# Optimization experiments

Measured on AMD Instinct MI355X. Metric: run time of the kernel, lower is better.

Reference implementation:

```python
import jax, jax.numpy as jnp
import numpy as np
from jax import lax

B, T = 32, 20
H, E, A, V = 256, 512, 256, 10000
GH, GW, D = 32, 32, 256          # info spatial grid and channel dim
P = GH * GW                      # num_pixels = 1024
IN_FLAT = P * D                  # 262144
REL = 128 * 128                  # 16384
LSTM_IN = E + D + H              # input to gate linears (x = [word, att_feat], then cat h)


def setup_inputs() -> dict:
    key = jax.random.key(0)
    ks = iter(jax.random.split(key, 40))
    def W(shape, scale=0.05):
        return jax.random.normal(next(ks), shape, jnp.float32) * scale
    inp = {}
    inp["info"] = jax.random.normal(next(ks), (B, GH, GW, D), jnp.float32)
    inp["relation"] = jax.random.normal(next(ks), (B, 128, 128), jnp.float32)
    inp["captions"] = jax.random.randint(next(ks), (B, T), 0, V)
    lens = jax.random.randint(next(ks), (B, 1), 5, T + 1).at[0, 0].set(T)
    inp["captions_lens"] = lens
    # embedding + attention
    inp["emb"] = W((V, E), 0.1)
    inp["W_enc"] = W((D, A)); inp["b_enc"] = jnp.zeros((A,), jnp.float32)
    inp["W_dec"] = W((H, A)); inp["b_dec"] = jnp.zeros((A,), jnp.float32)
    inp["W_full"] = W((A,));  inp["b_full"] = jnp.zeros((), jnp.float32)
    # MSLSTM cell (5 gate linears + mlp)
    for g in ("i", "f", "o", "g1", "g2"):
        inp[f"W_{g}"] = W((LSTM_IN, H)); inp[f"b_{g}"] = jnp.zeros((H,), jnp.float32)
    inp["W_mlp"] = W((2 * H, H)); inp["b_mlp"] = jnp.zeros((H,), jnp.float32)
    # f_beta, fc, init-state linears
    inp["W_beta"] = W((H, D)); inp["b_beta"] = jnp.zeros((D,), jnp.float32)
    inp["W_fc"] = W((H, V), 0.1); inp["b_fc"] = jnp.zeros((V,), jnp.float32)
    inp["W_ih"] = W((IN_FLAT, H), 0.005); inp["b_ih"] = jnp.zeros((H,), jnp.float32)
    inp["W_ic"] = W((IN_FLAT, H), 0.005); inp["b_ic"] = jnp.zeros((H,), jnp.float32)
    inp["W_iC"] = W((REL, H), 0.01);      inp["b_iC"] = jnp.zeros((H,), jnp.float32)
    return inp


def reference(info, relation, captions, captions_lens, emb,
              W_enc, b_enc, W_dec, b_dec, W_full, b_full,
              W_i, b_i, W_f, b_f, W_o, b_o, W_g1, b_g1, W_g2, b_g2,
              W_mlp, b_mlp, W_beta, b_beta, W_fc, b_fc,
              W_ih, b_ih, W_ic, b_ic, W_iC, b_iC):
    Bsz = captions.shape[0]
    info_f = info.reshape(Bsz, P, D)
    rel_f = relation.reshape(Bsz, REL)
    lens = captions_lens[:, 0]
    order = jnp.argsort(-lens)                      # sort descending by length
    lens = lens[order]
    caps = captions[order]
    info_f = info_f[order]
    rel_f = rel_f[order]
    sent_len = lens - 1
    Tm = captions.shape[1] - 1                      # static: max len forced to T in setup

    words = emb[caps]                               # (B, T, E)
    flat = info_f.reshape(Bsz, -1)                  # (B, P*D)
    h = flat @ W_ih + b_ih
    c = flat @ W_ic + b_ic
    C = rel_f @ W_iC + b_iC
    att1 = info_f @ W_enc + b_enc                   # (B, P, A) -- invariant over t

    def step(carry, xs):
        h, c, C = carry
        word, t = xs                                # word: (B, E)
        att2 = h @ W_dec + b_dec                    # (B, A)
        e = jax.nn.relu(att1 + att2[:, None, :]) @ W_full + b_full   # (B, P)
        alpha = jax.nn.softmax(e, axis=1)
        awf = jnp.einsum('bpd,bp->bd', info_f, alpha)                # (B, D)
        # note: gate=sigmoid(f_beta(h)) is computed in torch but its product is unused
        x = jnp.concatenate([word, awf, h], axis=1)  # cat([x, h]) with x=[word, awf]
        i = jax.nn.sigmoid(x @ W_i + b_i)
        f = jax.nn.sigmoid(x @ W_f + b_f)
        o = jax.nn.sigmoid(x @ W_o + b_o)
        g1 = jnp.tanh(x @ W_g1 + b_g1)
        g2 = jnp.tanh(x @ W_g2 + b_g2)
        new_c = f * c + i * g1
        new_C = f * C + i * g2
        new_h = o * jnp.tanh(jnp.concatenate([new_c, new_C], axis=1) @ W_mlp + b_mlp)
        pred = new_h @ W_fc + b_fc                  # dropout in eval mode = identity
        mask = (sent_len > t)[:, None].astype(pred.dtype)
        return (new_h, new_c, new_C), (pred * mask, alpha * mask)

    words_t = jnp.swapaxes(words[:, :Tm], 0, 1)     # (Tm, B, E)
    (_, (preds, alphas)) = lax.scan(step, (h, c, C), (words_t, jnp.arange(Tm)))
    predictions = jnp.swapaxes(preds, 0, 1)         # (B, Tm, V)
    alphas = jnp.swapaxes(alphas, 0, 1)             # (B, Tm, P)
    return predictions, alphas, order
```

## Files before the change

### kernel.cpp

```cpp
#include <hip/hip_runtime.h>
#include <math.h>

#define Bz 32
#define Tz 20
#define TMz 19
#define Vz 10000
#define INFLAT 262144
#define RELSZ 16384
#define NBLK 512

#define WS_PH     0
#define WS_PC     4194304
#define WS_ATT1H  0
#define WS_INFOH  4194304
#define WS_EXPE   8388608
#define WS_ZSUM   8421376
#define WS_AWF    8421888
#define WS_GSP    8430080
#define WS_HST    8593920
#define WS_CST0   8602112
#define WS_CSTB0  8610304
#define WS_CST1   8618496
#define WS_CSTB1  8626688
#define WS_AT2P   8634880
#define WS_INTS   8700416
#define WS_PCHC   8701440
#define WS_WG16   8701440
#define WS_WFC16  9750016
#define WS_END_WFC (9750016 + 1280000)

__device__ __forceinline__ float sigm(float x) { return 1.0f / (1.0f + expf(-x)); }

__device__ __forceinline__ unsigned short f2bf(float f) {
    unsigned int x = __float_as_uint(f);
    unsigned int r = (x + 0x7fffu + ((x >> 16) & 1u)) >> 16;
    return (unsigned short)r;
}
__device__ __forceinline__ float bfl(unsigned int u) { return __uint_as_float(u << 16); }
__device__ __forceinline__ float bfh(unsigned int u) { return __uint_as_float(u & 0xffff0000u); }

__device__ __forceinline__ float agload(const float* p) {
    return __hip_atomic_load(p, __ATOMIC_RELAXED, __HIP_MEMORY_SCOPE_AGENT);
}
__device__ __forceinline__ void agstore(float* p, float v) {
    __hip_atomic_store(p, v, __ATOMIC_RELAXED, __HIP_MEMORY_SCOPE_AGENT);
}
__device__ __forceinline__ int agloadi(const int* p) {
    return __hip_atomic_load(p, __ATOMIC_RELAXED, __HIP_MEMORY_SCOPE_AGENT);
}
__device__ __forceinline__ void agstorei(int* p, int v) {
    __hip_atomic_store(p, v, __ATOMIC_RELAXED, __HIP_MEMORY_SCOPE_AGENT);
}
__device__ __forceinline__ void agadd(float* p, float v) {
    __hip_atomic_fetch_add(p, v, __ATOMIC_RELAXED, __HIP_MEMORY_SCOPE_AGENT);
}

__device__ __forceinline__ void gbar(int* slots, int* root, int gen) {
    asm volatile("s_waitcnt vmcnt(0)" ::: "memory");
    __syncthreads();
    if (blockIdx.x == 0) {
        int i0 = threadIdx.x, i1 = threadIdx.x + 256;
        if (i0 != 0) {
            while (agloadi(&slots[i0]) < gen) __builtin_amdgcn_s_sleep(1);
        }
        while (agloadi(&slots[i1]) < gen) __builtin_amdgcn_s_sleep(1);
        __syncthreads();
        if (threadIdx.x == 0) agstorei(root, gen);
    } else if (threadIdx.x == 0) {
        agstorei(&slots[blockIdx.x], gen);
        while (agloadi(root) < gen) __builtin_amdgcn_s_sleep(2);
    }
    __syncthreads();
    asm volatile("" ::: "memory");
}

__global__ void k_sort(const int* __restrict__ lens, float* __restrict__ out_order,
                       int* __restrict__ ord, int* __restrict__ sentlen, int* __restrict__ barmem) {
    if (threadIdx.x == 0 && blockIdx.x == 0) {
        for (int i = 0; i < 64 + NBLK; ++i) barmem[i] = 0;
        int l[Bz]; bool used[Bz];
        for (int b = 0; b < Bz; ++b) { l[b] = lens[b]; used[b] = false; }
        for (int i = 0; i < Bz; ++i) {
            int best = -1;
            for (int j = 0; j < Bz; ++j)
                if (!used[j] && (best < 0 || l[j] > l[best])) best = j;
            used[best] = true;
            ord[i] = best;
            sentlen[i] = l[best] - 1;
            out_order[i] = (float)best;
        }
    }
}

__global__ __launch_bounds__(256) void k_gemv2(const float* __restrict__ X, const int* __restrict__ ord,
                                               const float* __restrict__ W1, const float* __restrict__ W2,
                                               float* __restrict__ p1, float* __restrict__ p2) {
    __shared__ __align__(16) float xsT[512 * 36];
    __shared__ int ords[32];
    int tid = threadIdx.x;
    size_t k0 = (size_t)blockIdx.x * 512;

    if (tid < 32) ords[tid] = ord[tid];
    __syncthreads();

    for (int idx = tid; idx < 4096; idx += 256) {
        int b = idx >> 7, kq = idx & 127;
        float4 v = *(const float4*)&X[(size_t)ords[b] * INFLAT + k0 + kq * 4];
        xsT[(kq * 4 + 0) * 36 + b] = v.x;
        xsT[(kq * 4 + 1) * 36 + b] = v.y;
        xsT[(kq * 4 + 2) * 36 + b] = v.z;
        xsT[(kq * 4 + 3) * 36 + b] = v.w;
    }
    __syncthreads();

    float ah[32], ac[32];
#pragma unroll
    for (int b = 0; b < 32; ++b) { ah[b] = 0.f; ac[b] = 0.f; }

    const float* w1p = W1 + k0 * 256 + tid;
    const float* w2p = W2 + k0 * 256 + tid;
#pragma unroll 4
    for (int k = 0; k < 512; ++k) {
        float w1 = w1p[(size_t)k * 256];
        float w2 = w2p[(size_t)k * 256];
        const float4* xr = (const float4*)&xsT[k * 36];
#pragma unroll
        for (int bq = 0; bq < 8; ++bq) {
            float4 x4 = xr[bq];
            ah[bq * 4 + 0] += x4.x * w1; ac[bq * 4 + 0] += x4.x * w2;
            ah[bq * 4 + 1] += x4.y * w1; ac[bq * 4 + 1] += x4.y * w2;
            ah[bq * 4 + 2] += x4.z * w1; ac[bq * 4 + 2] += x4.z * w2;
            ah[bq * 4 + 3] += x4.w * w1; ac[bq * 4 + 3] += x4.w * w2;
        }
    }
#pragma unroll
    for (int b = 0; b < 32; ++b) {
        size_t o = ((size_t)blockIdx.x * 32 + b) * 256 + tid;
        p1[o] = ah[b];
        p2[o] = ac[b];
    }
}

__global__ __launch_bounds__(256) void k_gemvC(const float* __restrict__ R, const int* __restrict__ ord,
                                               const float* __restrict__ W, float* __restrict__ p) {
    __shared__ float xs[32 * 128];
    __shared__ int ords[32];
    int tid = threadIdx.x, bx = blockIdx.x;
    if (tid < 32) ords[tid] = ord[tid];
    __syncthreads();
    int k0 = bx * 128;
    for (int idx = tid; idx < 32 * 128; idx += 256) {
        int b = idx >> 7, kk = idx & 127;
        xs[idx] = R[(size_t)ords[b] * RELSZ + k0 + kk];
    }
    __syncthreads();
    float acc[32];
#pragma unroll
    for (int b = 0; b < 32; ++b) acc[b] = 0.f;
    for (int kk = 0; kk < 128; ++kk) {
        float w = W[(size_t)(k0 + kk) * 256 + tid];
#pragma unroll
        for (int b = 0; b < 32; ++b) acc[b] += xs[b * 128 + kk] * w;
    }
#pragma unroll
    for (int b = 0; b < 32; ++b) p[((size_t)bx * 32 + b) * 256 + tid] = acc[b];
}

__global__ __launch_bounds__(256) void k_reduce3(const float* __restrict__ ph, const float* __restrict__ pc,
                                                 const float* __restrict__ pC,
                                                 const float* __restrict__ b_ih, const float* __restrict__ b_ic,
                                                 const float* __restrict__ b_iC,
                                                 float* __restrict__ hst, float* __restrict__ cst,
                                                 float* __restrict__ Cst) {
    int which = blockIdx.x >> 5, b = blockIdx.x & 31, j = threadIdx.x;
    if (which == 0) {
        float s0 = b_ih[j], s1 = 0.f, s2 = 0.f, s3 = 0.f;
        for (int c = 0; c < 512; c += 4) {
            s0 += ph[((size_t)((c + 0) * 32 + b)) * 256 + j];
            s1 += ph[((size_t)((c + 1) * 32 + b)) * 256 + j];
            s2 += ph[((size_t)((c + 2) * 32 + b)) * 256 + j];
            s3 += ph[((size_t)((c + 3) * 32 + b)) * 256 + j];
        }
        hst[b * 256 + j] = s0 + s1 + s2 + s3;
    } else if (which == 1) {
        float s0 = b_ic[j], s1 = 0.f, s2 = 0.f, s3 = 0.f;
        for (int c = 0; c < 512; c += 4) {
            s0 += pc[((size_t)((c + 0) * 32 + b)) * 256 + j];
            s1 += pc[((size_t)((c + 1) * 32 + b)) * 256 + j];
            s2 += pc[((size_t)((c + 2) * 32 + b)) * 256 + j];
            s3 += pc[((size_t)((c + 3) * 32 + b)) * 256 + j];
        }
        cst[b * 256 + j] = s0 + s1 + s2 + s3;
    } else {
        float s0 = b_iC[j], s1 = 0.f, s2 = 0.f, s3 = 0.f;
        for (int c = 0; c < 128; c += 4) {
            s0 += pC[((size_t)((c + 0) * 32 + b)) * 256 + j];
            s1 += pC[((size_t)((c + 1) * 32 + b)) * 256 + j];
            s2 += pC[((size_t)((c + 2) * 32 + b)) * 256 + j];
            s3 += pC[((size_t)((c + 3) * 32 + b)) * 256 + j];
        }
        Cst[b * 256 + j] = s0 + s1 + s2 + s3;
    }
}

__global__ __launch_bounds__(256) void k_init2(const float* __restrict__ hst, const float* __restrict__ W_dec,
                                               float* __restrict__ at2p, float* __restrict__ awf,
                                               float* __restrict__ zsum) {
    __shared__ __align__(16) float hs[8192];
    int tid = threadIdx.x;
    for (int i = blockIdx.x * 256 + tid; i < 8192; i += 1024) awf[i] = 0.f;
    if (blockIdx.x == 0 && tid < 32) zsum[tid] = 0.f;
    for (int i = tid; i < 2048; i += 256) ((float4*)hs)[i] = ((const float4*)hst)[i];
    __syncthreads();
    int col = blockIdx.x * 64 + (tid & 63), bg = tid >> 6;
    float acc[8] = {0.f,0.f,0.f,0.f,0.f,0.f,0.f,0.f};
    for (int k = 0; k < 256; ++k) {
        float w = W_dec[(size_t)k * 256 + col];
#pragma unroll
        for (int bi = 0; bi < 8; ++bi) acc[bi] += hs[(bg * 8 + bi) * 256 + k] * w;
    }
#pragma unroll
    for (int bi = 0; bi < 8; ++bi) {
        int b = bg * 8 + bi;
        at2p[((size_t)(b * 8 + 0)) * 256 + col] = acc[bi];
#pragma unroll
        for (int ct = 1; ct < 8; ++ct) at2p[((size_t)(b * 8 + ct)) * 256 + col] = 0.f;
    }
}

__global__ __launch_bounds__(256) void k_wfc16(const float* __restrict__ W_fc,
                                               unsigned short* __restrict__ wfcT16) {
    __shared__ unsigned short tile[16 * 256];
    int tid = threadIdx.x;
    int c0 = blockIdx.x * 16;
    for (int p = 0; p < 16; ++p) {
        int r = p * 16 + (tid >> 4);
        int c = tid & 15;
        tile[c * 256 + r] = f2bf(W_fc[(size_t)r * Vz + c0 + c]);
    }
    __syncthreads();
    unsigned int* dst = (unsigned int*)wfcT16 + (size_t)c0 * 128;
    const unsigned int* src = (const unsigned int*)tile;
    for (int i = tid; i < 2048; i += 256) dst[i] = src[i];
}

__global__ __launch_bounds__(256) void k_wg16(const float* __restrict__ W_i, const float* __restrict__ W_f,
                                              const float* __restrict__ W_o, const float* __restrict__ W_g1,
                                              const float* __restrict__ W_g2,
                                              unsigned short* __restrict__ wg16) {
    __shared__ unsigned short tile[16 * 1024];
    int tid = threadIdx.x;
    int g = blockIdx.x >> 4;
    int c0 = (blockIdx.x & 15) * 16;
    const float* Wg = (g == 0) ? W_i : (g == 1) ? W_f : (g == 2) ? W_o : (g == 3) ? W_g1 : W_g2;
    for (int p = 0; p < 64; ++p) {
        int r = p * 16 + (tid >> 4);
        int c = tid & 15;
        tile[c * 1024 + r] = f2bf(Wg[(size_t)r * 256 + c0 + c]);
    }
    __syncthreads();
    unsigned int* dst = (unsigned int*)wg16 + ((size_t)(g * 256 + c0)) * 512;
    const unsigned int* src = (const unsigned int*)tile;
    for (int i = tid; i < 8192; i += 256) dst[i] = src[i];
}

__global__ __launch_bounds__(256) void k_att1(const float* __restrict__ info, const int* __restrict__ ord,
                                              const float* __restrict__ W, const float* __restrict__ bias,
                                              unsigned short* __restrict__ att1h,
                                              unsigned short* __restrict__ infoh) {
    __shared__ __align__(16) float xsT[256 * 36];
    int tid = threadIdx.x;
    int r0 = blockIdx.x * 32;
    int b = r0 >> 10, p0 = r0 & 1023;
    const float* src = info + (size_t)ord[b] * INFLAT + (size_t)p0 * 256;
    for (int idx = tid; idx < 2048; idx += 256) {
        int r = idx >> 6, kq = idx & 63;
        float4 v = *(const float4*)&src[r * 256 + kq * 4];
        xsT[(kq * 4 + 0) * 36 + r] = v.x;
        xsT[(kq * 4 + 1) * 36 + r] = v.y;
        xsT[(kq * 4 + 2) * 36 + r] = v.z;
        xsT[(kq * 4 + 3) * 36 + r] = v.w;
    }
    __syncthreads();
#pragma unroll 4
    for (int r = 0; r < 32; ++r)
        infoh[(size_t)(r0 + r) * 256 + tid] = f2bf(xsT[tid * 36 + r]);
    float acc[32];
#pragma unroll
    for (int r = 0; r < 32; ++r) acc[r] = 0.f;
    for (int k = 0; k < 256; ++k) {
        float w = W[k * 256 + tid];
        const float4* xr = (const float4*)&xsT[k * 36];
#pragma unroll
        for (int rq = 0; rq < 8; ++rq) {
            float4 x4 = xr[rq];
            acc[rq * 4 + 0] += x4.x * w;
            acc[rq * 4 + 1] += x4.y * w;
            acc[rq * 4 + 2] += x4.z * w;
            acc[rq * 4 + 3] += x4.w * w;
        }
    }
    float bj = bias[tid];
#pragma unroll
    for (int r = 0; r < 32; ++r)
        att1h[(size_t)(r0 + r) * 256 + tid] = f2bf(acc[r] + bj);
}

struct KArgs {
    const float *info, *emb, *W_dec, *b_dec, *W_full, *b_full;
    const float *b_i, *b_f, *b_o, *b_g1, *b_g2;
    const float *W_mlp, *b_mlp, *W_fc, *b_fc;
    const int *caps;
    const unsigned short *att1h, *infoh, *wfcT16, *wg16;
    float *expe, *zsum, *awf, *gsp, *hst, *cst0, *Cst0, *cst1, *Cst1, *at2p;
    const int *ord, *slp;
    int *root, *slots;
    float *out_pred, *out_alpha;
};

__device__ void pred_task2(const KArgs& a, unsigned short* hb, int tile, int tm1) {
    int tid = threadIdx.x;
    for (int i = tid; i < 8192; i += 256) hb[i] = f2bf(agload(&a.hst[i]));
    __syncthreads();
    int col = tile * 64 + (tid & 63), bg = tid >> 6;
    if (col >= Vz) return;
    float acc[8] = {0.f, 0.f, 0.f, 0.f, 0.f, 0.f, 0.f, 0.f};
    if (a.wfcT16) {
        const uint4* wcol = (const uint4*)(a.wfcT16 + (size_t)col * 256);
#pragma unroll 4
        for (int q = 0; q < 32; ++q) {
            uint4 u = wcol[q];
            float w0 = bfl(u.x), w1 = bfh(u.x), w2 = bfl(u.y), w3 = bfh(u.y);
            float w4 = bfl(u.z), w5 = bfh(u.z), w6 = bfl(u.w), w7 = bfh(u.w);
#pragma unroll
            for (int bi = 0; bi < 8; ++bi) {
                uint4 hv = *(const uint4*)&hb[(bg * 8 + bi) * 256 + q * 8];
                acc[bi] += bfl(hv.x) * w0 + bfh(hv.x) * w1 + bfl(hv.y) * w2 + bfh(hv.y) * w3
                         + bfl(hv.z) * w4 + bfh(hv.z) * w5 + bfl(hv.w) * w6 + bfh(hv.w) * w7;
            }
        }
    } else {
        for (int jq = 0; jq < 64; ++jq) {
            float w0 = a.W_fc[(size_t)(jq * 4 + 0) * Vz + col];
            float w1 = a.W_fc[(size_t)(jq * 4 + 1) * Vz + col];
            float w2 = a.W_fc[(size_t)(jq * 4 + 2) * Vz + col];
            float w3 = a.W_fc[(size_t)(jq * 4 + 3) * Vz + col];
#pragma unroll
            for (int bi = 0; bi < 8; ++bi) {
                uint2 u = *(const uint2*)&hb[(bg * 8 + bi) * 256 + jq * 4];
                acc[bi] += bfl(u.x) * w0 + bfh(u.x) * w1 + bfl(u.y) * w2 + bfh(u.y) * w3;
            }
        }
    }
    float bv = a.b_fc[col];
#pragma unroll
    for (int bi = 0; bi < 8; ++bi) {
        int b = bg * 8 + bi;
        float r = (a.slp[b] > tm1) ? (acc[bi] + bv) : 0.f;
        a.out_pred[((size_t)b * TMz + tm1) * Vz + col] = r;
    }
}

__global__ __launch_bounds__(256, 2) void k_steps(KArgs a) {
    __shared__ __align__(16) unsigned char smem[81920];
    unsigned char* attB = smem;
    unsigned char* infB = smem + 32768;
    float* F = (float*)(smem + 65536);
    unsigned short* S16 = (unsigned short*)(smem + 65536);

    int bid = blockIdx.x, tid = threadIdx.x;
    int b = bid >> 4, sub = bid & 15;
    int gen = 0;

    {
        const unsigned short* ag = a.att1h + (size_t)(b * 1024 + sub * 64) * 256;
        const unsigned short* ig = a.infoh + (size_t)(b * 1024 + sub * 64) * 256;
        for (int idx = tid; idx < 2048; idx += 256) {
            int r = idx >> 5, qc = idx & 31;
            uint4 v = *(const uint4*)(ag + (size_t)r * 256 + qc * 8);
            *(uint4*)(attB + r * 512 + ((qc ^ (r & 7)) << 4)) = v;
            uint4 w2 = *(const uint4*)(ig + (size_t)r * 256 + qc * 8);
            *(uint4*)(infB + idx * 16) = w2;
        }
    }
    __syncthreads();

    for (int t = 0; t < TMz; ++t) {
        {
            float v = a.b_dec[tid];
#pragma unroll
            for (int ct = 0; ct < 8; ++ct) v += agload(&a.at2p[((size_t)(b * 8 + ct)) * 256 + tid]);
            F[tid] = v;
            F[256 + tid] = a.W_full[tid];
            __syncthreads();
            int pl = tid & 63, kq = tid >> 6;
            float part = 0.f;
#pragma unroll
            for (int q = 0; q < 8; ++q) {
                int c = kq * 8 + q;
                uint4 u = *(const uint4*)(attB + pl * 512 + ((c ^ (pl & 7)) << 4));
                const float* A = F + kq * 64 + q * 8;
                const float* W = F + 256 + kq * 64 + q * 8;
                part += fmaxf(bfl(u.x) + A[0], 0.f) * W[0];
                part += fmaxf(bfh(u.x) + A[1], 0.f) * W[1];
                part += fmaxf(bfl(u.y) + A[2], 0.f) * W[2];
                part += fmaxf(bfh(u.y) + A[3], 0.f) * W[3];
                part += fmaxf(bfl(u.z) + A[4], 0.f) * W[4];
                part += fmaxf(bfh(u.z) + A[5], 0.f) * W[5];
                part += fmaxf(bfl(u.w) + A[6], 0.f) * W[6];
                part += fmaxf(bfh(u.w) + A[7], 0.f) * W[7];
            }
            F[512 + kq * 64 + pl] = part;
            __syncthreads();
            if (tid < 64) {
                float e = F[512 + tid] + F[576 + tid] + F[640 + tid] + F[704 + tid] + a.b_full[0];
                float ex = expf(e);
                agstore(&a.expe[b * 1024 + sub * 64 + tid], ex);
                F[768 + tid] = ex;
                float s = ex;
                s += __shfl_down(s, 32); s += __shfl_down(s, 16); s += __shfl_down(s, 8);
                s += __shfl_down(s, 4);  s += __shfl_down(s, 2);  s += __shfl_down(s, 1);
                if (tid == 0) agadd(&a.zsum[b], s);
            }
            __syncthreads();
            int gg = tid >> 7, c2 = tid & 127;
            const unsigned char* ib = infB + gg * 512 + c2 * 4;
            const float* ex = F + 768;
            float a0 = 0.f, a1 = 0.f;
#pragma unroll
            for (int i = 0; i < 32; ++i) {
                unsigned int u = *(const unsigned int*)(ib + i * 1024);
                float ev = ex[i * 2 + gg];
                a0 += ev * bfl(u);
                a1 += ev * bfh(u);
            }
            F[832 + gg * 256 + c2 * 2]     = a0;
            F[832 + gg * 256 + c2 * 2 + 1] = a1;
            __syncthreads();
            agadd(&a.awf[b * 256 + tid], F[832 + tid] + F[1088 + tid]);
        }
        gbar(a.slots, a.root, ++gen);

        if (bid < 80) {
            int g = bid / 16, s16 = bid % 16;
            int ct = s16 >> 2, kc = s16 & 3;
            for (int idx = tid; idx < 8192; idx += 256) {
                int b2 = idx >> 8, kk = idx & 255;
                float v;
                if (kc == 0) {
                    int cap = a.caps[a.ord[b2] * Tz + t];
                    v = a.emb[(size_t)cap * 512 + kk];
                } else if (kc == 1) {
                    int cap = a.caps[a.ord[b2] * Tz + t];
                    v = a.emb[(size_t)cap * 512 + 256 + kk];
                } else if (kc == 2) {
                    v = agload(&a.awf[b2 * 256 + kk]);
                } else {
                    v = agload(&a.hst[b2 * 256 + kk]);
                }
                S16[idx] = f2bf(v);
            }
            __syncthreads();
            int col = ct * 64 + (tid & 63), bg = tid >> 6;
            const uint4* wcol = (const uint4*)(a.wg16 + ((size_t)(g * 256 + col)) * 1024 + kc * 256);
            float acc[8] = {0.f,0.f,0.f,0.f,0.f,0.f,0.f,0.f};
#pragma unroll 4
            for (int q = 0; q < 32; ++q) {
                uint4 u = wcol[q];
                float w0 = bfl(u.x), w1 = bfh(u.x), w2 = bfl(u.y), w3 = bfh(u.y);
                float w4 = bfl(u.z), w5 = bfh(u.z), w6 = bfl(u.w), w7 = bfh(u.w);
#pragma unroll
                for (int bi = 0; bi < 8; ++bi) {
                    uint4 xv = *(const uint4*)&S16[(bg * 8 + bi) * 256 + q * 8];
                    acc[bi] += bfl(xv.x) * w0 + bfh(xv.x) * w1 + bfl(xv.y) * w2 + bfh(xv.y) * w3
                             + bfl(xv.z) * w4 + bfh(xv.z) * w5 + bfl(xv.w) * w6 + bfh(xv.w) * w7;
                }
            }
            if (kc == 2) {
#pragma unroll
                for (int bi = 0; bi < 8; ++bi) {
                    float Z = agload(&a.zsum[bg * 8 + bi]);
                    acc[bi] *= (1.0f / Z);
                }
            }
#pragma unroll
            for (int bi = 0; bi < 8; ++bi)
                agstore(&a.gsp[((size_t)((g * 4 + kc) * 32 + bg * 8 + bi)) * 256 + col], acc[bi]);
        } else if (bid < 237) {
            if (bid < 112) {
                int bb = bid - 80;
                float Z = agload(&a.zsum[bb]);
                float invZ = 1.0f / Z;
                float am = (a.slp[bb] > t) ? invZ : 0.f;
                float* oal = a.out_alpha + ((size_t)bb * TMz + t) * 1024;
                for (int p = tid; p < 1024; p += 256) oal[p] = agload(&a.expe[bb * 1024 + p]) * am;
            }
            if (t > 0) pred_task2(a, S16, bid - 80, t - 1);
        }
        gbar(a.slots, a.root, ++gen);

        if (bid < 256) {
            int bb = bid >> 3, ct = bid & 7;
            int j = tid;
            const float* csOld = (t & 1) ? a.cst1 : a.cst0;
            const float* CsOld = (t & 1) ? a.Cst1 : a.Cst0;
            float* csNew = (t & 1) ? a.cst0 : a.cst1;
            float* CsNew = (t & 1) ? a.Cst0 : a.Cst1;
            float gs[5];
#pragma unroll
            for (int g = 0; g < 5; ++g) {
                float s = 0.f;
#pragma unroll
                for (int kc = 0; kc < 4; ++kc)
                    s += agload(&a.gsp[((size_t)((g * 4 + kc) * 32 + bb)) * 256 + j]);
                gs[g] = s;
            }
            gs[0] += a.b_i[j]; gs[1] += a.b_f[j]; gs[2] += a.b_o[j];
            gs[3] += a.b_g1[j]; gs[4] += a.b_g2[j];
            float iv = sigm(gs[0]), fv = sigm(gs[1]), ov = sigm(gs[2]);
            float g1 = tanhf(gs[3]), g2 = tanhf(gs[4]);
            float nc = fv * agload(&csOld[bb * 256 + j]) + iv * g1;
            float nC = fv * agload(&CsOld[bb * 256 + j]) + iv * g2;
            if (ct == 0) {
                agstore(&csNew[bb * 256 + j], nc);
                agstore(&CsNew[bb * 256 + j], nC);
            }
            if (ct == 1 && tid == 0) agstore(&a.zsum[bb], 0.f);
            F[j] = nc;
            F[256 + j] = nC;
            F[512 + j] = ov;
            __syncthreads();
            int colL = tid & 31, kth = tid >> 5;
            int col = ct * 32 + colL;
            float part = 0.f;
            const float* wm = a.W_mlp + col;
            for (int i = 0; i < 64; ++i) {
                int k = kth * 64 + i;
                part += F[k] * wm[(size_t)k * 256];
            }
            F[768 + colL * 9 + kth] = part;
            __syncthreads();
            if (tid < 32) {
                int c2 = ct * 32 + tid;
                float m = a.b_mlp[c2];
#pragma unroll
                for (int kk = 0; kk < 8; ++kk) m += F[768 + tid * 9 + kk];
                float hv = F[512 + c2] * tanhf(m);
                agstore(&a.hst[bb * 256 + c2], hv);
                F[1056 + tid] = hv;
                agstore(&a.awf[bb * 256 + c2], 0.f);
            }
            __syncthreads();
            float acc = 0.f;
            const float* wd = a.W_dec + (size_t)(ct * 32) * 256 + tid;
#pragma unroll
            for (int kk = 0; kk < 32; ++kk) acc += F[1056 + kk] * wd[(size_t)kk * 256];
            agstore(&a.at2p[((size_t)(bb * 8 + ct)) * 256 + tid], acc);
        }
        gbar(a.slots, a.root, ++gen);
    }

    if (bid >= 80 && bid < 237) pred_task2(a, S16, bid - 80, TMz - 1);
}

extern "C" void kernel_launch(void* const* d_in, const int* in_sizes, int n_in,
                              void* d_out, int out_size, void* d_ws, size_t ws_size,
                              hipStream_t stream) {
    const float* info  = (const float*)d_in[0];
    const float* rel   = (const float*)d_in[1];
    const int*   caps  = (const int*)d_in[2];
    const int*   lens  = (const int*)d_in[3];
    const float* emb   = (const float*)d_in[4];
    const float* W_enc = (const float*)d_in[5];
    const float* b_enc = (const float*)d_in[6];
    const float* W_dec = (const float*)d_in[7];
    const float* b_dec = (const float*)d_in[8];
    const float* W_full= (const float*)d_in[9];
    const float* b_full= (const float*)d_in[10];
    const float* W_i   = (const float*)d_in[11];
    const float* b_i   = (const float*)d_in[12];
    const float* W_f   = (const float*)d_in[13];
    const float* b_f   = (const float*)d_in[14];
    const float* W_o   = (const float*)d_in[15];
    const float* b_o   = (const float*)d_in[16];
    const float* W_g1  = (const float*)d_in[17];
    const float* b_g1  = (const float*)d_in[18];
    const float* W_g2  = (const float*)d_in[19];
    const float* b_g2  = (const float*)d_in[20];
    const float* W_mlp = (const float*)d_in[21];
    const float* b_mlp = (const float*)d_in[22];
    const float* W_fc  = (const float*)d_in[25];
    const float* b_fc  = (const float*)d_in[26];
    const float* W_ih  = (const float*)d_in[27];
    const float* b_ih  = (const float*)d_in[28];
    const float* W_ic  = (const float*)d_in[29];
    const float* b_ic  = (const float*)d_in[30];
    const float* W_iC  = (const float*)d_in[31];
    const float* b_iC  = (const float*)d_in[32];

    float* out = (float*)d_out;
    float* out_pred  = out;
    float* out_alpha = out + (size_t)Bz * TMz * Vz;
    float* out_order = out_alpha + (size_t)Bz * TMz * 1024;

    float* w = (float*)d_ws;
    float* ph   = w + WS_PH;
    float* pcp  = w + WS_PC;
    unsigned short* att1h = (unsigned short*)(w + WS_ATT1H);
    unsigned short* infoh = (unsigned short*)(w + WS_INFOH);
    float* expe = w + WS_EXPE;
    float* zsum = w + WS_ZSUM;
    float* awf  = w + WS_AWF;
    float* gsp  = w + WS_GSP;
    float* hst  = w + WS_HST;
    float* cst0 = w + WS_CST0;
    float* Cst0 = w + WS_CSTB0;
    float* cst1 = w + WS_CST1;
    float* Cst1 = w + WS_CSTB1;
    float* at2p = w + WS_AT2P;
    int*   ordp = (int*)(w + WS_INTS);
    int*   slp  = ordp + 32;
    int*   barmem = ordp + 64;
    float* pC   = w + WS_PCHC;
    unsigned short* wg16   = (unsigned short*)(w + WS_WG16);
    unsigned short* wfcT16 = (unsigned short*)(w + WS_WFC16);

    int useWfc = (ws_size >= (size_t)WS_END_WFC * 4);

    k_sort<<<1, 64, 0, stream>>>(lens, out_order, ordp, slp, barmem);
    k_gemv2<<<512, 256, 0, stream>>>(info, ordp, W_ih, W_ic, ph, pcp);
    k_gemvC<<<128, 256, 0, stream>>>(rel, ordp, W_iC, pC);
    k_reduce3<<<96, 256, 0, stream>>>(ph, pcp, pC, b_ih, b_ic, b_iC, hst, cst0, Cst0);
    k_init2<<<4, 256, 0, stream>>>(hst, W_dec, at2p, awf, zsum);
    k_wg16<<<80, 256, 0, stream>>>(W_i, W_f, W_o, W_g1, W_g2, wg16);
    if (useWfc) k_wfc16<<<625, 256, 0, stream>>>(W_fc, wfcT16);
    k_att1<<<1024, 256, 0, stream>>>(info, ordp, W_enc, b_enc, att1h, infoh);

    KArgs ka;
    ka.info = info; ka.emb = emb; ka.W_dec = W_dec; ka.b_dec = b_dec;
    ka.W_full = W_full; ka.b_full = b_full;
    ka.b_i = b_i; ka.b_f = b_f; ka.b_o = b_o; ka.b_g1 = b_g1; ka.b_g2 = b_g2;
    ka.W_mlp = W_mlp; ka.b_mlp = b_mlp; ka.W_fc = W_fc; ka.b_fc = b_fc;
    ka.caps = caps;
    ka.att1h = att1h; ka.infoh = infoh;
    ka.wfcT16 = useWfc ? wfcT16 : (const unsigned short*)0;
    ka.wg16 = wg16;
    ka.expe = expe; ka.zsum = zsum; ka.awf = awf;
    ka.gsp = gsp; ka.hst = hst;
    ka.cst0 = cst0; ka.Cst0 = Cst0; ka.cst1 = cst1; ka.Cst1 = Cst1;
    ka.at2p = at2p;
    ka.ord = ordp; ka.slp = slp;
    ka.root = barmem; ka.slots = barmem + 64;
    ka.out_pred = out_pred; ka.out_alpha = out_alpha;

    k_steps<<<NBLK, 256, 0, stream>>>(ka);
}
```

Baseline: 1.950 ms.

## Replace grid-barrier persistent kernel with per-batch independent blocks

The persistent 512-block kernel, which needed three global barriers per timestep, is replaced by a 64-block kernel of 1024 threads. Each pair of blocks owns one batch element and runs the whole recurrence locally in shared memory: attention, gates, MLP and W_dec. The pair splits only the vocabulary projection between its two blocks. This removes grid-wide synchronisation and the global scratch traffic for partial sums. In exchange, both blocks of a pair compute the recurrence redundantly, only 64 CUs are used, and each block streams the gate and fc weights from cache every step. Gate weights, W_fc and info are now stored in fp16 and consumed with fdot2 instructions instead of bf16 unpacking.

```diff
diff --git a/kernel.cpp b/kernel.cpp
--- a/kernel.cpp
+++ b/kernel.cpp
@@ -7,28 +7,22 @@
 #define Vz 10000
 #define INFLAT 262144
 #define RELSZ 16384
-#define NBLK 512
 
 #define WS_PH     0
 #define WS_PC     4194304
 #define WS_ATT1H  0
 #define WS_INFOH  4194304
-#define WS_EXPE   8388608
-#define WS_ZSUM   8421376
-#define WS_AWF    8421888
-#define WS_GSP    8430080
 #define WS_HST    8593920
 #define WS_CST0   8602112
 #define WS_CSTB0  8610304
-#define WS_CST1   8618496
-#define WS_CSTB1  8626688
-#define WS_AT2P   8634880
 #define WS_INTS   8700416
 #define WS_PCHC   8701440
 #define WS_WG16   8701440
 #define WS_WFC16  9750016
 #define WS_END_WFC (9750016 + 1280000)
 
+typedef _Float16 half2_t __attribute__((ext_vector_type(2)));
+
 __device__ __forceinline__ float sigm(float x) { return 1.0f / (1.0f + expf(-x)); }
 
 __device__ __forceinline__ unsigned short f2bf(float f) {
@@ -39,45 +33,17 @@
 __device__ __forceinline__ float bfl(unsigned int u) { return __uint_as_float(u << 16); }
 __device__ __forceinline__ float bfh(unsigned int u) { return __uint_as_float(u & 0xffff0000u); }
 
-__device__ __forceinline__ float agload(const float* p) {
-    return __hip_atomic_load(p, __ATOMIC_RELAXED, __HIP_MEMORY_SCOPE_AGENT);
-}
-__device__ __forceinline__ void agstore(float* p, float v) {
-    __hip_atomic_store(p, v, __ATOMIC_RELAXED, __HIP_MEMORY_SCOPE_AGENT);
-}
-__device__ __forceinline__ int agloadi(const int* p) {
-    return __hip_atomic_load(p, __ATOMIC_RELAXED, __HIP_MEMORY_SCOPE_AGENT);
-}
-__device__ __forceinline__ void agstorei(int* p, int v) {
-    __hip_atomic_store(p, v, __ATOMIC_RELAXED, __HIP_MEMORY_SCOPE_AGENT);
-}
-__device__ __forceinline__ void agadd(float* p, float v) {
-    __hip_atomic_fetch_add(p, v, __ATOMIC_RELAXED, __HIP_MEMORY_SCOPE_AGENT);
-}
-
-__device__ __forceinline__ void gbar(int* slots, int* root, int gen) {
-    asm volatile("s_waitcnt vmcnt(0)" ::: "memory");
-    __syncthreads();
-    if (blockIdx.x == 0) {
-        int i0 = threadIdx.x, i1 = threadIdx.x + 256;
-        if (i0 != 0) {
-            while (agloadi(&slots[i0]) < gen) __builtin_amdgcn_s_sleep(1);
-        }
-        while (agloadi(&slots[i1]) < gen) __builtin_amdgcn_s_sleep(1);
-        __syncthreads();
-        if (threadIdx.x == 0) agstorei(root, gen);
-    } else if (threadIdx.x == 0) {
-        agstorei(&slots[blockIdx.x], gen);
-        while (agloadi(root) < gen) __builtin_amdgcn_s_sleep(2);
-    }
-    __syncthreads();
-    asm volatile("" ::: "memory");
+__device__ __forceinline__ unsigned short f2h(float f) {
+    _Float16 h = (_Float16)f;
+    return *(unsigned short*)&h;
+}
+__device__ __forceinline__ half2_t u2h2(unsigned int v) {
+    union { unsigned int u; half2_t h; } x; x.u = v; return x.h;
 }
 
 __global__ void k_sort(const int* __restrict__ lens, float* __restrict__ out_order,
-                       int* __restrict__ ord, int* __restrict__ sentlen, int* __restrict__ barmem) {
+                       int* __restrict__ ord, int* __restrict__ sentlen) {
     if (threadIdx.x == 0 && blockIdx.x == 0) {
-        for (int i = 0; i < 64 + NBLK; ++i) barmem[i] = 0;
         int l[Bz]; bool used[Bz];
         for (int b = 0; b < Bz; ++b) { l[b] = lens[b]; used[b] = false; }
         for (int i = 0; i < Bz; ++i) {
@@ -203,31 +169,6 @@
     }
 }
 
-__global__ __launch_bounds__(256) void k_init2(const float* __restrict__ hst, const float* __restrict__ W_dec,
-                                               float* __restrict__ at2p, float* __restrict__ awf,
-                                               float* __restrict__ zsum) {
-    __shared__ __align__(16) float hs[8192];
-    int tid = threadIdx.x;
-    for (int i = blockIdx.x * 256 + tid; i < 8192; i += 1024) awf[i] = 0.f;
-    if (blockIdx.x == 0 && tid < 32) zsum[tid] = 0.f;
-    for (int i = tid; i < 2048; i += 256) ((float4*)hs)[i] = ((const float4*)hst)[i];
-    __syncthreads();
-    int col = blockIdx.x * 64 + (tid & 63), bg = tid >> 6;
-    float acc[8] = {0.f,0.f,0.f,0.f,0.f,0.f,0.f,0.f};
-    for (int k = 0; k < 256; ++k) {
-        float w = W_dec[(size_t)k * 256 + col];
-#pragma unroll
-        for (int bi = 0; bi < 8; ++bi) acc[bi] += hs[(bg * 8 + bi) * 256 + k] * w;
-    }
-#pragma unroll
-    for (int bi = 0; bi < 8; ++bi) {
-        int b = bg * 8 + bi;
-        at2p[((size_t)(b * 8 + 0)) * 256 + col] = acc[bi];
-#pragma unroll
-        for (int ct = 1; ct < 8; ++ct) at2p[((size_t)(b * 8 + ct)) * 256 + col] = 0.f;
-    }
-}
-
 __global__ __launch_bounds__(256) void k_wfc16(const float* __restrict__ W_fc,
                                                unsigned short* __restrict__ wfcT16) {
     __shared__ unsigned short tile[16 * 256];
@@ -236,7 +177,7 @@
     for (int p = 0; p < 16; ++p) {
         int r = p * 16 + (tid >> 4);
         int c = tid & 15;
-        tile[c * 256 + r] = f2bf(W_fc[(size_t)r * Vz + c0 + c]);
+        tile[c * 256 + r] = f2h(W_fc[(size_t)r * Vz + c0 + c]);
     }
     __syncthreads();
     unsigned int* dst = (unsigned int*)wfcT16 + (size_t)c0 * 128;
@@ -256,7 +197,7 @@
     for (int p = 0; p < 64; ++p) {
         int r = p * 16 + (tid >> 4);
         int c = tid & 15;
-        tile[c * 1024 + r] = f2bf(Wg[(size_t)r * 256 + c0 + c]);
+        tile[c * 1024 + r] = f2h(Wg[(size_t)r * 256 + c0 + c]);
     }
     __syncthreads();
     unsigned int* dst = (unsigned int*)wg16 + ((size_t)(g * 256 + c0)) * 512;
@@ -284,7 +225,7 @@
     __syncthreads();
 #pragma unroll 4
     for (int r = 0; r < 32; ++r)
-        infoh[(size_t)(r0 + r) * 256 + tid] = f2bf(xsT[tid * 36 + r]);
+        infoh[(size_t)(r0 + r) * 256 + tid] = f2h(xsT[tid * 36 + r]);
     float acc[32];
 #pragma unroll
     for (int r = 0; r < 32; ++r) acc[r] = 0.f;
@@ -307,260 +248,242 @@
 }
 
 struct KArgs {
-    const float *info, *emb, *W_dec, *b_dec, *W_full, *b_full;
+    const float *emb, *W_dec, *b_dec, *W_full, *b_full;
     const float *b_i, *b_f, *b_o, *b_g1, *b_g2;
     const float *W_mlp, *b_mlp, *W_fc, *b_fc;
     const int *caps;
     const unsigned short *att1h, *infoh, *wfcT16, *wg16;
-    float *expe, *zsum, *awf, *gsp, *hst, *cst0, *Cst0, *cst1, *Cst1, *at2p;
+    const float *hst, *cst0, *Cst0;
     const int *ord, *slp;
-    int *root, *slots;
     float *out_pred, *out_alpha;
 };
 
-__device__ void pred_task2(const KArgs& a, unsigned short* hb, int tile, int tm1) {
-    int tid = threadIdx.x;
-    for (int i = tid; i < 8192; i += 256) hb[i] = f2bf(agload(&a.hst[i]));
-    __syncthreads();
-    int col = tile * 64 + (tid & 63), bg = tid >> 6;
-    if (col >= Vz) return;
-    float acc[8] = {0.f, 0.f, 0.f, 0.f, 0.f, 0.f, 0.f, 0.f};
-    if (a.wfcT16) {
-        const uint4* wcol = (const uint4*)(a.wfcT16 + (size_t)col * 256);
+__global__ __launch_bounds__(1024, 1) void k_batch(KArgs a) {
+    __shared__ float hs[256], cs[256], Cs[256], at2[256], wfv[256], aw[256], ovs[256];
+    __shared__ float ex[1024];
+    __shared__ float part[2080];
+    __shared__ float gs[1280];
+    __shared__ __align__(16) unsigned short x16[1024];
+    __shared__ __align__(16) unsigned short h16[256];
+    __shared__ float Zs;
+
+    int bid = blockIdx.x, tid = threadIdx.x;
+    int b = bid >> 1, rep = bid & 1;
+    int ordb = a.ord[b];
+    int sl = a.slp[b];
+    float bfull = a.b_full[0];
+
+    if (tid < 256) {
+        hs[tid] = a.hst[b * 256 + tid];
+        cs[tid] = a.cst0[b * 256 + tid];
+        Cs[tid] = a.Cst0[b * 256 + tid];
+        wfv[tid] = a.W_full[tid];
+    }
+    __syncthreads();
+
+    const unsigned short* attB = a.att1h + (size_t)b * 1024 * 256;
+    const unsigned short* infB = a.infoh + (size_t)b * 1024 * 256;
+
+    for (int t = 0; t < TMz; ++t) {
+        {
+            int j = tid & 255, q = tid >> 8;
+            float s = 0.f;
+            const float* wd = a.W_dec + (size_t)(q * 64) * 256 + j;
+            for (int k = 0; k < 64; ++k) s += hs[q * 64 + k] * wd[(size_t)k * 256];
+            part[q * 256 + j] = s;
+        }
+        __syncthreads();
+        if (tid < 256) at2[tid] = a.b_dec[tid] + part[tid] + part[256 + tid] + part[512 + tid] + part[768 + tid];
+        __syncthreads();
+
+        {
+            int sub = tid & 3, pr = tid >> 2;
+#pragma unroll 1
+            for (int pass = 0; pass < 4; ++pass) {
+                int p = pass * 256 + pr;
+                const uint4* row = (const uint4*)(attB + (size_t)p * 256);
+                float s = 0.f;
+#pragma unroll
+                for (int c = 0; c < 8; ++c) {
+                    int ui = c * 4 + sub;
+                    uint4 u = row[ui];
+                    const float* A = at2 + ui * 8;
+                    const float* W = wfv + ui * 8;
+                    s += fmaxf(bfl(u.x) + A[0], 0.f) * W[0] + fmaxf(bfh(u.x) + A[1], 0.f) * W[1]
+                       + fmaxf(bfl(u.y) + A[2], 0.f) * W[2] + fmaxf(bfh(u.y) + A[3], 0.f) * W[3]
+                       + fmaxf(bfl(u.z) + A[4], 0.f) * W[4] + fmaxf(bfh(u.z) + A[5], 0.f) * W[5]
+                       + fmaxf(bfl(u.w) + A[6], 0.f) * W[6] + fmaxf(bfh(u.w) + A[7], 0.f) * W[7];
+                }
+                s += __shfl_xor(s, 1);
+                s += __shfl_xor(s, 2);
+                if (sub == 0) ex[p] = expf(s + bfull);
+            }
+        }
+        __syncthreads();
+
+        if (tid < 256) part[tid] = ex[tid] + ex[256 + tid] + ex[512 + tid] + ex[768 + tid];
+        __syncthreads();
+        if (tid < 32) {
+            float s = 0.f;
+#pragma unroll
+            for (int k = 0; k < 8; ++k) s += part[tid * 8 + k];
+            part[2048 + tid] = s;
+        }
+        __syncthreads();
+        if (tid == 0) {
+            float s = 0.f;
+#pragma unroll
+            for (int k = 0; k < 32; ++k) s += part[2048 + k];
+            Zs = s;
+        }
+        __syncthreads();
+        float invZ = 1.0f / Zs;
+
+        if (rep == 0) {
+            float am = (sl > t) ? invZ : 0.f;
+            a.out_alpha[((size_t)b * TMz + t) * 1024 + tid] = ex[tid] * am;
+        }
+
+        {
+            int dp = tid & 127, q = tid >> 7;
+            int d0 = dp * 2;
+            const unsigned short* ib = infB + (size_t)(q * 128) * 256 + d0;
+            float a0 = 0.f, a1 = 0.f;
+            for (int p = 0; p < 128; ++p) {
+                unsigned int u = *(const unsigned int*)(ib + (size_t)p * 256);
+                half2_t hp = u2h2(u);
+                float ev = ex[q * 128 + p];
+                a0 += ev * (float)hp.x;
+                a1 += ev * (float)hp.y;
+            }
+            part[q * 256 + d0] = a0;
+            part[q * 256 + d0 + 1] = a1;
+        }
+        __syncthreads();
+        if (tid < 256) {
+            float s = 0.f;
+#pragma unroll
+            for (int q = 0; q < 8; ++q) s += part[q * 256 + tid];
+            aw[tid] = s * invZ;
+        }
+        __syncthreads();
+
+        {
+            int cap = a.caps[ordb * Tz + t];
+            float v;
+            if (tid < 512) v = a.emb[(size_t)cap * 512 + tid];
+            else if (tid < 768) v = aw[tid - 512];
+            else v = hs[tid - 768];
+            x16[tid] = f2h(v);
+        }
+        __syncthreads();
+
+        {
+            int sub = tid & 3, j = tid >> 2;
+            const uint4* xr = (const uint4*)x16;
+#pragma unroll 1
+            for (int g = 0; g < 5; ++g) {
+                const uint4* wcol = (const uint4*)(a.wg16 + ((size_t)(g * 256 + j)) * 1024);
+                float s = 0.f;
 #pragma unroll 4
-        for (int q = 0; q < 32; ++q) {
-            uint4 u = wcol[q];
-            float w0 = bfl(u.x), w1 = bfh(u.x), w2 = bfl(u.y), w3 = bfh(u.y);
-            float w4 = bfl(u.z), w5 = bfh(u.z), w6 = bfl(u.w), w7 = bfh(u.w);
-#pragma unroll
-            for (int bi = 0; bi < 8; ++bi) {
-                uint4 hv = *(const uint4*)&hb[(bg * 8 + bi) * 256 + q * 8];
-                acc[bi] += bfl(hv.x) * w0 + bfh(hv.x) * w1 + bfl(hv.y) * w2 + bfh(hv.y) * w3
-                         + bfl(hv.z) * w4 + bfh(hv.z) * w5 + bfl(hv.w) * w6 + bfh(hv.w) * w7;
-            }
-        }
-    } else {
-        for (int jq = 0; jq < 64; ++jq) {
-            float w0 = a.W_fc[(size_t)(jq * 4 + 0) * Vz + col];
-            float w1 = a.W_fc[(size_t)(jq * 4 + 1) * Vz + col];
-            float w2 = a.W_fc[(size_t)(jq * 4 + 2) * Vz + col];
-            float w3 = a.W_fc[(size_t)(jq * 4 + 3) * Vz + col];
-#pragma unroll
-            for (int bi = 0; bi < 8; ++bi) {
-                uint2 u = *(const uint2*)&hb[(bg * 8 + bi) * 256 + jq * 4];
-                acc[bi] += bfl(u.x) * w0 + bfh(u.x) * w1 + bfl(u.y) * w2 + bfh(u.y) * w3;
-            }
-        }
-    }
-    float bv = a.b_fc[col];
-#pragma unroll
-    for (int bi = 0; bi < 8; ++bi) {
-        int b = bg * 8 + bi;
-        float r = (a.slp[b] > tm1) ? (acc[bi] + bv) : 0.f;
-        a.out_pred[((size_t)b * TMz + tm1) * Vz + col] = r;
-    }
-}
-
-__global__ __launch_bounds__(256, 2) void k_steps(KArgs a) {
-    __shared__ __align__(16) unsigned char smem[81920];
-    unsigned char* attB = smem;
-    unsigned char* infB = smem + 32768;
-    float* F = (float*)(smem + 65536);
-    unsigned short* S16 = (unsigned short*)(smem + 65536);
-
-    int bid = blockIdx.x, tid = threadIdx.x;
-    int b = bid >> 4, sub = bid & 15;
-    int gen = 0;
-
-    {
-        const unsigned short* ag = a.att1h + (size_t)(b * 1024 + sub * 64) * 256;
-        const unsigned short* ig = a.infoh + (size_t)(b * 1024 + sub * 64) * 256;
-        for (int idx = tid; idx < 2048; idx += 256) {
-            int r = idx >> 5, qc = idx & 31;
-            uint4 v = *(const uint4*)(ag + (size_t)r * 256 + qc * 8);
-            *(uint4*)(attB + r * 512 + ((qc ^ (r & 7)) << 4)) = v;
-            uint4 w2 = *(const uint4*)(ig + (size_t)r * 256 + qc * 8);
-            *(uint4*)(infB + idx * 16) = w2;
-        }
-    }
-    __syncthreads();
-
-    for (int t = 0; t < TMz; ++t) {
-        {
-            float v = a.b_dec[tid];
-#pragma unroll
-            for (int ct = 0; ct < 8; ++ct) v += agload(&a.at2p[((size_t)(b * 8 + ct)) * 256 + tid]);
-            F[tid] = v;
-            F[256 + tid] = a.W_full[tid];
-            __syncthreads();
-            int pl = tid & 63, kq = tid >> 6;
-            float part = 0.f;
-#pragma unroll
-            for (int q = 0; q < 8; ++q) {
-                int c = kq * 8 + q;
-                uint4 u = *(const uint4*)(attB + pl * 512 + ((c ^ (pl & 7)) << 4));
-                const float* A = F + kq * 64 + q * 8;
-                const float* W = F + 256 + kq * 64 + q * 8;
-                part += fmaxf(bfl(u.x) + A[0], 0.f) * W[0];
-                part += fmaxf(bfh(u.x) + A[1], 0.f) * W[1];
-                part += fmaxf(bfl(u.y) + A[2], 0.f) * W[2];
-                part += fmaxf(bfh(u.y) + A[3], 0.f) * W[3];
-                part += fmaxf(bfl(u.z) + A[4], 0.f) * W[4];
-                part += fmaxf(bfh(u.z) + A[5], 0.f) * W[5];
-                part += fmaxf(bfl(u.w) + A[6], 0.f) * W[6];
-                part += fmaxf(bfh(u.w) + A[7], 0.f) * W[7];
-            }
-            F[512 + kq * 64 + pl] = part;
-            __syncthreads();
-            if (tid < 64) {
-                float e = F[512 + tid] + F[576 + tid] + F[640 + tid] + F[704 + tid] + a.b_full[0];
-                float ex = expf(e);
-                agstore(&a.expe[b * 1024 + sub * 64 + tid], ex);
-                F[768 + tid] = ex;
-                float s = ex;
-                s += __shfl_down(s, 32); s += __shfl_down(s, 16); s += __shfl_down(s, 8);
-                s += __shfl_down(s, 4);  s += __shfl_down(s, 2);  s += __shfl_down(s, 1);
-                if (tid == 0) agadd(&a.zsum[b], s);
-            }
-            __syncthreads();
-            int gg = tid >> 7, c2 = tid & 127;
-            const unsigned char* ib = infB + gg * 512 + c2 * 4;
-            const float* ex = F + 768;
-            float a0 = 0.f, a1 = 0.f;
-#pragma unroll
-            for (int i = 0; i < 32; ++i) {
-                unsigned int u = *(const unsigned int*)(ib + i * 1024);
-                float ev = ex[i * 2 + gg];
-                a0 += ev * bfl(u);
-                a1 += ev * bfh(u);
-            }
-            F[832 + gg * 256 + c2 * 2]     = a0;
-            F[832 + gg * 256 + c2 * 2 + 1] = a1;
-            __syncthreads();
-            agadd(&a.awf[b * 256 + tid], F[832 + tid] + F[1088 + tid]);
-        }
-        gbar(a.slots, a.root, ++gen);
-
-        if (bid < 80) {
-            int g = bid / 16, s16 = bid % 16;
-            int ct = s16 >> 2, kc = s16 & 3;
-            for (int idx = tid; idx < 8192; idx += 256) {
-                int b2 = idx >> 8, kk = idx & 255;
-                float v;
-                if (kc == 0) {
-                    int cap = a.caps[a.ord[b2] * Tz + t];
-                    v = a.emb[(size_t)cap * 512 + kk];
-                } else if (kc == 1) {
-                    int cap = a.caps[a.ord[b2] * Tz + t];
-                    v = a.emb[(size_t)cap * 512 + 256 + kk];
-                } else if (kc == 2) {
-                    v = agload(&a.awf[b2 * 256 + kk]);
-                } else {
-                    v = agload(&a.hst[b2 * 256 + kk]);
+                for (int c = 0; c < 32; ++c) {
+                    int ui = c * 4 + sub;
+                    uint4 w = wcol[ui];
+                    uint4 x = xr[ui];
+                    s = __builtin_amdgcn_fdot2(u2h2(w.x), u2h2(x.x), s, false);
+                    s = __builtin_amdgcn_fdot2(u2h2(w.y), u2h2(x.y), s, false);
+                    s = __builtin_amdgcn_fdot2(u2h2(w.z), u2h2(x.z), s, false);
+                    s = __builtin_amdgcn_fdot2(u2h2(w.w), u2h2(x.w), s, false);
                 }
-                S16[idx] = f2bf(v);
-            }
-            __syncthreads();
-            int col = ct * 64 + (tid & 63), bg = tid >> 6;
-            const uint4* wcol = (const uint4*)(a.wg16 + ((size_t)(g * 256 + col)) * 1024 + kc * 256);
-            float acc[8] = {0.f,0.f,0.f,0.f,0.f,0.f,0.f,0.f};
-#pragma unroll 4
-            for (int q = 0; q < 32; ++q) {
-                uint4 u = wcol[q];
-                float w0 = bfl(u.x), w1 = bfh(u.x), w2 = bfl(u.y), w3 = bfh(u.y);
-                float w4 = bfl(u.z), w5 = bfh(u.z), w6 = bfl(u.w), w7 = bfh(u.w);
-#pragma unroll
-                for (int bi = 0; bi < 8; ++bi) {
-                    uint4 xv = *(const uint4*)&S16[(bg * 8 + bi) * 256 + q * 8];
-                    acc[bi] += bfl(xv.x) * w0 + bfh(xv.x) * w1 + bfl(xv.y) * w2 + bfh(xv.y) * w3
-                             + bfl(xv.z) * w4 + bfh(xv.z) * w5 + bfl(xv.w) * w6 + bfh(xv.w) * w7;
+                s += __shfl_xor(s, 1);
+                s += __shfl_xor(s, 2);
+                if (sub == 0) {
+                    const float* bb = (g == 0) ? a.b_i : (g == 1) ? a.b_f : (g == 2) ? a.b_o : (g == 3) ? a.b_g1 : a.b_g2;
+                    gs[g * 256 + j] = bb[j] + s;
                 }
             }
-            if (kc == 2) {
-#pragma unroll
-                for (int bi = 0; bi < 8; ++bi) {
-                    float Z = agload(&a.zsum[bg * 8 + bi]);
-                    acc[bi] *= (1.0f / Z);
+        }
+        __syncthreads();
+
+        if (tid < 256) {
+            float iv = sigm(gs[tid]), fv = sigm(gs[256 + tid]), ov = sigm(gs[512 + tid]);
+            float g1 = tanhf(gs[768 + tid]), g2 = tanhf(gs[1024 + tid]);
+            float nc = fv * cs[tid] + iv * g1;
+            float nC = fv * Cs[tid] + iv * g2;
+            cs[tid] = nc; Cs[tid] = nC;
+            part[tid] = nc; part[256 + tid] = nC;
+            ovs[tid] = ov;
+        }
+        __syncthreads();
+
+        {
+            int j = tid & 255, q = tid >> 8;
+            float s = 0.f;
+            const float* wm = a.W_mlp + (size_t)(q * 128) * 256 + j;
+            for (int k = 0; k < 128; ++k) s += part[q * 128 + k] * wm[(size_t)k * 256];
+            part[1024 + q * 256 + j] = s;
+        }
+        __syncthreads();
+        if (tid < 256) {
+            float m = a.b_mlp[tid] + part[1024 + tid] + part[1280 + tid] + part[1536 + tid] + part[1792 + tid];
+            float hv = ovs[tid] * tanhf(m);
+            hs[tid] = hv;
+            h16[tid] = f2h(hv);
+        }
+        __syncthreads();
+
+        {
+            bool on = (sl > t);
+            float* op = a.out_pred + ((size_t)b * TMz + t) * Vz;
+            if (a.wfcT16) {
+                int sub = tid & 3, cr = tid >> 2;
+                const uint4* hr = (const uint4*)h16;
+#pragma unroll 1
+                for (int pass = 0; pass < 20; ++pass) {
+                    int cid = pass * 256 + cr;
+                    int col = rep * 5000 + cid;
+                    float s = 0.f;
+                    if (cid < 5000) {
+                        const uint4* wcol = (const uint4*)(a.wfcT16 + (size_t)col * 256);
+#pragma unroll
+                        for (int c = 0; c < 8; ++c) {
+                            int ui = c * 4 + sub;
+                            uint4 w = wcol[ui];
+                            uint4 h = hr[ui];
+                            s = __builtin_amdgcn_fdot2(u2h2(w.x), u2h2(h.x), s, false);
+                            s = __builtin_amdgcn_fdot2(u2h2(w.y), u2h2(h.y), s, false);
+                            s = __builtin_amdgcn_fdot2(u2h2(w.z), u2h2(h.z), s, false);
+                            s = __builtin_amdgcn_fdot2(u2h2(w.w), u2h2(h.w), s, false);
+                        }
+                    }
+                    s += __shfl_xor(s, 1);
+                    s += __shfl_xor(s, 2);
+                    if (sub == 0 && cid < 5000)
+                        op[col] = on ? (s + a.b_fc[col]) : 0.f;
+                }
+            } else {
+                float acc[5] = {0.f, 0.f, 0.f, 0.f, 0.f};
+                for (int k = 0; k < 256; ++k) {
+                    float hv = hs[k];
+                    const float* wr = a.W_fc + (size_t)k * Vz + rep * 5000;
+#pragma unroll
+                    for (int uu = 0; uu < 5; ++uu) {
+                        int cid = uu * 1024 + tid;
+                        if (cid < 5000) acc[uu] += hv * wr[cid];
+                    }
+                }
+#pragma unroll
+                for (int uu = 0; uu < 5; ++uu) {
+                    int cid = uu * 1024 + tid;
+                    if (cid < 5000) {
+                        int col = rep * 5000 + cid;
+                        op[col] = on ? (acc[uu] + a.b_fc[col]) : 0.f;
+                    }
                 }
             }
-#pragma unroll
-            for (int bi = 0; bi < 8; ++bi)
-                agstore(&a.gsp[((size_t)((g * 4 + kc) * 32 + bg * 8 + bi)) * 256 + col], acc[bi]);
-        } else if (bid < 237) {
-            if (bid < 112) {
-                int bb = bid - 80;
-                float Z = agload(&a.zsum[bb]);
-                float invZ = 1.0f / Z;
-                float am = (a.slp[bb] > t) ? invZ : 0.f;
-                float* oal = a.out_alpha + ((size_t)bb * TMz + t) * 1024;
-                for (int p = tid; p < 1024; p += 256) oal[p] = agload(&a.expe[bb * 1024 + p]) * am;
-            }
-            if (t > 0) pred_task2(a, S16, bid - 80, t - 1);
-        }
-        gbar(a.slots, a.root, ++gen);
-
-        if (bid < 256) {
-            int bb = bid >> 3, ct = bid & 7;
-            int j = tid;
-            const float* csOld = (t & 1) ? a.cst1 : a.cst0;
-            const float* CsOld = (t & 1) ? a.Cst1 : a.Cst0;
-            float* csNew = (t & 1) ? a.cst0 : a.cst1;
-            float* CsNew = (t & 1) ? a.Cst0 : a.Cst1;
-            float gs[5];
-#pragma unroll
-            for (int g = 0; g < 5; ++g) {
-                float s = 0.f;
-#pragma unroll
-                for (int kc = 0; kc < 4; ++kc)
-                    s += agload(&a.gsp[((size_t)((g * 4 + kc) * 32 + bb)) * 256 + j]);
-                gs[g] = s;
-            }
-            gs[0] += a.b_i[j]; gs[1] += a.b_f[j]; gs[2] += a.b_o[j];
-            gs[3] += a.b_g1[j]; gs[4] += a.b_g2[j];
-            float iv = sigm(gs[0]), fv = sigm(gs[1]), ov = sigm(gs[2]);
-            float g1 = tanhf(gs[3]), g2 = tanhf(gs[4]);
-            float nc = fv * agload(&csOld[bb * 256 + j]) + iv * g1;
-            float nC = fv * agload(&CsOld[bb * 256 + j]) + iv * g2;
-            if (ct == 0) {
-                agstore(&csNew[bb * 256 + j], nc);
-                agstore(&CsNew[bb * 256 + j], nC);
-            }
-            if (ct == 1 && tid == 0) agstore(&a.zsum[bb], 0.f);
-            F[j] = nc;
-            F[256 + j] = nC;
-            F[512 + j] = ov;
-            __syncthreads();
-            int colL = tid & 31, kth = tid >> 5;
-            int col = ct * 32 + colL;
-            float part = 0.f;
-            const float* wm = a.W_mlp + col;
-            for (int i = 0; i < 64; ++i) {
-                int k = kth * 64 + i;
-                part += F[k] * wm[(size_t)k * 256];
-            }
-            F[768 + colL * 9 + kth] = part;
-            __syncthreads();
-            if (tid < 32) {
-                int c2 = ct * 32 + tid;
-                float m = a.b_mlp[c2];
-#pragma unroll
-                for (int kk = 0; kk < 8; ++kk) m += F[768 + tid * 9 + kk];
-                float hv = F[512 + c2] * tanhf(m);
-                agstore(&a.hst[bb * 256 + c2], hv);
-                F[1056 + tid] = hv;
-                agstore(&a.awf[bb * 256 + c2], 0.f);
-            }
-            __syncthreads();
-            float acc = 0.f;
-            const float* wd = a.W_dec + (size_t)(ct * 32) * 256 + tid;
-#pragma unroll
-            for (int kk = 0; kk < 32; ++kk) acc += F[1056 + kk] * wd[(size_t)kk * 256];
-            agstore(&a.at2p[((size_t)(bb * 8 + ct)) * 256 + tid], acc);
-        }
-        gbar(a.slots, a.root, ++gen);
-    }
-
-    if (bid >= 80 && bid < 237) pred_task2(a, S16, bid - 80, TMz - 1);
+        }
+        __syncthreads();
+    }
 }
 
 extern "C" void kernel_launch(void* const* d_in, const int* in_sizes, int n_in,
@@ -608,36 +531,27 @@
     float* pcp  = w + WS_PC;
     unsigned short* att1h = (unsigned short*)(w + WS_ATT1H);
     unsigned short* infoh = (unsigned short*)(w + WS_INFOH);
-    float* expe = w + WS_EXPE;
-    float* zsum = w + WS_ZSUM;
-    float* awf  = w + WS_AWF;
-    float* gsp  = w + WS_GSP;
     float* hst  = w + WS_HST;
     float* cst0 = w + WS_CST0;
     float* Cst0 = w + WS_CSTB0;
-    float* cst1 = w + WS_CST1;
-    float* Cst1 = w + WS_CSTB1;
-    float* at2p = w + WS_AT2P;
     int*   ordp = (int*)(w + WS_INTS);
     int*   slp  = ordp + 32;
-    int*   barmem = ordp + 64;
     float* pC   = w + WS_PCHC;
     unsigned short* wg16   = (unsigned short*)(w + WS_WG16);
     unsigned short* wfcT16 = (unsigned short*)(w + WS_WFC16);
 
     int useWfc = (ws_size >= (size_t)WS_END_WFC * 4);
 
-    k_sort<<<1, 64, 0, stream>>>(lens, out_order, ordp, slp, barmem);
+    k_sort<<<1, 64, 0, stream>>>(lens, out_order, ordp, slp);
     k_gemv2<<<512, 256, 0, stream>>>(info, ordp, W_ih, W_ic, ph, pcp);
     k_gemvC<<<128, 256, 0, stream>>>(rel, ordp, W_iC, pC);
     k_reduce3<<<96, 256, 0, stream>>>(ph, pcp, pC, b_ih, b_ic, b_iC, hst, cst0, Cst0);
-    k_init2<<<4, 256, 0, stream>>>(hst, W_dec, at2p, awf, zsum);
     k_wg16<<<80, 256, 0, stream>>>(W_i, W_f, W_o, W_g1, W_g2, wg16);
     if (useWfc) k_wfc16<<<625, 256, 0, stream>>>(W_fc, wfcT16);
     k_att1<<<1024, 256, 0, stream>>>(info, ordp, W_enc, b_enc, att1h, infoh);
 
     KArgs ka;
-    ka.info = info; ka.emb = emb; ka.W_dec = W_dec; ka.b_dec = b_dec;
+    ka.emb = emb; ka.W_dec = W_dec; ka.b_dec = b_dec;
     ka.W_full = W_full; ka.b_full = b_full;
     ka.b_i = b_i; ka.b_f = b_f; ka.b_o = b_o; ka.b_g1 = b_g1; ka.b_g2 = b_g2;
     ka.W_mlp = W_mlp; ka.b_mlp = b_mlp; ka.W_fc = W_fc; ka.b_fc = b_fc;
@@ -645,13 +559,9 @@
     ka.att1h = att1h; ka.infoh = infoh;
     ka.wfcT16 = useWfc ? wfcT16 : (const unsigned short*)0;
     ka.wg16 = wg16;
-    ka.expe = expe; ka.zsum = zsum; ka.awf = awf;
-    ka.gsp = gsp; ka.hst = hst;
-    ka.cst0 = cst0; ka.Cst0 = Cst0; ka.cst1 = cst1; ka.Cst1 = Cst1;
-    ka.at2p = at2p;
+    ka.hst = hst; ka.cst0 = cst0; ka.Cst0 = Cst0;
     ka.ord = ordp; ka.slp = slp;
-    ka.root = barmem; ka.slots = barmem + 64;
     ka.out_pred = out_pred; ka.out_alpha = out_alpha;
 
-    k_steps<<<NBLK, 256, 0, stream>>>(ka);
-}
+    k_batch<<<64, 1024, 0, stream>>>(ka);
+}
```

Result: slower. 4.252 ms (+118.0%).
